# Performance work log

Measured on AMD Instinct MI355X. Metric: run time of the kernel, lower is better.

## Reference

```python
import jax, jax.numpy as jnp
import numpy as np

E = 1024   # embedding_dim
H = 16     # num_head
D = 64     # dim_head (E == H*D)
R = 8      # LoRA rank
BATCH = 2
SEQ = 2048
EPS = 1e-6


def setup_inputs() -> dict:
    key = jax.random.key(0)
    ks = jax.random.split(key, 16)
    s = 0.02
    return {
        "y": jax.random.normal(ks[0], (BATCH, SEQ, E), jnp.float32),
        "Wqkv": jax.random.normal(ks[1], (3 * E, E), jnp.float32) * s,
        "bqkv": jax.random.normal(ks[2], (3 * E,), jnp.float32) * s,
        "Wmsa": jax.random.normal(ks[3], (E, E), jnp.float32) * s,
        "Bq": jax.random.normal(ks[4], (E, R), jnp.float32) * s,
        "Aq": jax.random.normal(ks[5], (R, E), jnp.float32) * s,
        "Bk": jax.random.normal(ks[6], (E, R), jnp.float32) * s,
        "Ak": jax.random.normal(ks[7], (R, E), jnp.float32) * s,
        "Bv": jax.random.normal(ks[8], (E, R), jnp.float32) * s,
        "Av": jax.random.normal(ks[9], (R, E), jnp.float32) * s,
        "Bo": jax.random.normal(ks[10], (E, R), jnp.float32) * s,
        "Ao": jax.random.normal(ks[11], (R, E), jnp.float32) * s,
        "gamma": jnp.ones((E,), jnp.float32),
        "beta": jnp.zeros((E,), jnp.float32),
        "i": 0,
    }


def reference(y, Wqkv, bqkv, Wmsa, Bq, Aq, Bk, Ak, Bv, Av, Bo, Ao, gamma, beta, i):
    B, S, En = y.shape
    # fused QKV projection: nn.Linear -> y @ W.T + b
    qkv = (y @ Wqkv.T + bqkv).reshape(B, S, 3, H, D).transpose(2, 0, 3, 1, 4)
    Q, K, V = qkv[0], qkv[1], qkv[2]          # each [B,H,S,D]

    def lora_delta(Bw, Aw):
        # torch: y @ (B.weight @ A.weight), reshaped to heads
        return (y @ (Bw @ Aw)).reshape(B, S, H, D).transpose(0, 2, 1, 3)

    Q = Q + lora_delta(Bq, Aq)
    K = K + lora_delta(Bk, Ak)
    V = V + lora_delta(Bv, Av)

    scale = jnp.asarray(np.sqrt(D), y.dtype)
    scores = jnp.einsum('bhqd,bhkd->bhqk', Q, K) / scale
    attn = jax.nn.softmax(scores, axis=-1)
    o = jnp.einsum('bhqk,bhkd->bhqd', attn, V)          # [B,H,S,D]
    o = o.transpose(0, 2, 1, 3).reshape(B, S, H * D)    # [B,S,E]

    msa = o @ Wmsa.T + o @ (Bo @ Ao)
    res = msa + y

    mu = jnp.mean(res, axis=-1, keepdims=True)
    var = jnp.var(res, axis=-1, keepdims=True)
    return (res - mu) * jax.lax.rsqrt(var + EPS) * gamma + beta
```

## Files before the change

kernel.cpp:

```cpp
#include <hip/hip_runtime.h>
#include <hip/hip_bf16.h>
#include <stdint.h>

typedef __attribute__((ext_vector_type(8))) short short8;
typedef __attribute__((ext_vector_type(4))) float f32x4;

typedef const __attribute__((address_space(1))) void gv_t;
typedef __attribute__((address_space(3))) void lv_t;

#define SCQ 0.18033688011112042f

__device__ __forceinline__ void gl_lds16(const void* g, void* l) {
    __builtin_amdgcn_global_load_lds((gv_t*)g, (lv_t*)l, 16, 0, 0);
}

__device__ __forceinline__ unsigned short f2bf(float f) {
    union { float f; unsigned int u; } v; v.f = f;
    unsigned int r = v.u + 0x7fffu + ((v.u >> 16) & 1u);
    return (unsigned short)(r >> 16);
}

__device__ __forceinline__ unsigned int pack2bf(float a, float b) {
    union { __hip_bfloat162 h2; unsigned int u; } cv;
    cv.h2 = __float22bfloat162_rn(make_float2(a, b));
    return cv.u;
}

__device__ __forceinline__ f32x4 zero4() { f32x4 z = {0.f, 0.f, 0.f, 0.f}; return z; }

__global__ void k_prep(const float* __restrict__ y,
                       const float* __restrict__ Wqkv, const float* __restrict__ Wmsa,
                       const float* __restrict__ Bq, const float* __restrict__ Aq,
                       const float* __restrict__ Bk, const float* __restrict__ Ak,
                       const float* __restrict__ Bv, const float* __restrict__ Av,
                       const float* __restrict__ Bo, const float* __restrict__ Ao,
                       unsigned short* __restrict__ wout, unsigned short* __restrict__ yb) {
    const int bid = blockIdx.x;
    if (bid < 16384) {
        int idx = bid * 256 + threadIdx.x;
        int n = idx >> 10, k = idx & 1023;
        int sel = n >> 10, n0 = n & 1023;
        const float* Bp = (sel == 0) ? Bq : (sel == 1) ? Bk : (sel == 2) ? Bv : Bo;
        const float* Ap = (sel == 0) ? Aq : (sel == 1) ? Ak : (sel == 2) ? Av : Ao;
        float acc = (sel < 3) ? Wqkv[idx] : Wmsa[idx - 3145728];
        #pragma unroll
        for (int r = 0; r < 8; ++r) acc += Bp[k * 8 + r] * Ap[r * 1024 + n0];
        wout[idx] = f2bf(acc * ((sel == 0) ? SCQ : 1.0f));
    } else {
        int i = ((bid - 16384) * 256 + threadIdx.x) * 4;
        float4 v = *(const float4*)(y + i);
        union { unsigned short u[4]; uint2 w; } o;
        o.u[0] = f2bf(v.x); o.u[1] = f2bf(v.y); o.u[2] = f2bf(v.z); o.u[3] = f2bf(v.w);
        *(uint2*)(yb + i) = o.w;
    }
}

template <int TM, int EPI, int MINW>
__global__ __launch_bounds__(256, MINW) void k_gemm(const unsigned short* __restrict__ Ag,
                                                    const unsigned short* __restrict__ Bg,
                                                    const float* __restrict__ bias,
                                                    const float* __restrict__ yres,
                                                    unsigned short* __restrict__ vtg,
                                                    void* __restrict__ Cout,
                                                    int M, int N, int K) {
    constexpr int WAVES_N = 256 / TM;
    constexpr int WN = TM / 2;
    constexpr int NI = WN / 16;
    constexpr int ACALLS = TM / 64;
    __shared__ unsigned short As[2][TM * 32];
    __shared__ unsigned short Bs[2][128 * 32];
    const int flat = threadIdx.x;
    const int m0 = blockIdx.y * TM, n0 = blockIdx.x * 128;
    const int lane = flat & 63, wave = flat >> 6;
    const int l16 = lane & 15, quad = lane >> 4;
    const int wm = (wave / WAVES_N) * 64, wn = (wave % WAVES_N) * WN;

    f32x4 acc[4][NI];
    #pragma unroll
    for (int mi = 0; mi < 4; ++mi)
        #pragma unroll
        for (int ni = 0; ni < NI; ++ni) acc[mi][ni] = zero4();

    const unsigned short* ap = Ag + (size_t)(m0 + (flat >> 2)) * K + (flat & 3) * 8;
    const unsigned short* bp = Bg + (size_t)(n0 + (flat >> 2)) * K + (flat & 3) * 8;
    const size_t rstep = (size_t)64 * K;

    #pragma unroll
    for (int c = 0; c < ACALLS; ++c) gl_lds16(ap + c * rstep, &As[0][c * 2048 + flat * 8]);
    gl_lds16(bp,         &Bs[0][flat * 8]);
    gl_lds16(bp + rstep, &Bs[0][2048 + flat * 8]);
    ap += 32; bp += 32;
    __syncthreads();

    for (int k0 = 0; k0 < K; k0 += 32) {
        const int cur = (k0 >> 5) & 1;
        if (k0 + 32 < K) {
            const int nxt = cur ^ 1;
            #pragma unroll
            for (int c = 0; c < ACALLS; ++c) gl_lds16(ap + c * rstep, &As[nxt][c * 2048 + flat * 8]);
            gl_lds16(bp,         &Bs[nxt][flat * 8]);
            gl_lds16(bp + rstep, &Bs[nxt][2048 + flat * 8]);
            ap += 32; bp += 32;
        }

        short8 af[4], bfr[NI];
        #pragma unroll
        for (int i = 0; i < 4; ++i) af[i] = *(const short8*)&As[cur][(wm + i * 16 + l16) * 32 + quad * 8];
        #pragma unroll
        for (int i = 0; i < NI; ++i) bfr[i] = *(const short8*)&Bs[cur][(wn + i * 16 + l16) * 32 + quad * 8];
        #pragma unroll
        for (int mi = 0; mi < 4; ++mi)
            #pragma unroll
            for (int ni = 0; ni < NI; ++ni)
                acc[mi][ni] = __builtin_amdgcn_mfma_f32_16x16x32_bf16(af[mi], bfr[ni], acc[mi][ni], 0, 0, 0);

        __syncthreads();
    }

    if (EPI == 0) {
        unsigned short* C = (unsigned short*)Cout;
        if (n0 < 2048) {
            #pragma unroll
            for (int ni = 0; ni < NI; ++ni) {
                int col = n0 + wn + ni * 16 + l16;
                float bv = bias[col] * ((col < 1024) ? SCQ : 1.0f);
                #pragma unroll
                for (int mi = 0; mi < 4; ++mi) {
                    int row = m0 + wm + mi * 16 + quad * 4;
                    #pragma unroll
                    for (int r = 0; r < 4; ++r)
                        C[(size_t)(row + r) * N + col] = f2bf(acc[mi][ni][r] + bv);
                }
            }
        } else {
            #pragma unroll
            for (int ni = 0; ni < NI; ++ni) {
                int col = n0 + wn + ni * 16 + l16;
                float bv = bias[col];
                int hh = (col - 2048) >> 6, dd = col & 63;
                unsigned short* vrow0 = vtg + (size_t)(hh * 64 + dd) * 2048;
                #pragma unroll
                for (int mi = 0; mi < 4; ++mi) {
                    int row = m0 + wm + mi * 16 + quad * 4;
                    int bb = row >> 11, ss = row & 2047;
                    uint2 w;
                    w.x = pack2bf(acc[mi][ni][0] + bv, acc[mi][ni][1] + bv);
                    w.y = pack2bf(acc[mi][ni][2] + bv, acc[mi][ni][3] + bv);
                    *(uint2*)(vrow0 + (size_t)bb * 2097152 + ss) = w;
                }
            }
        }
    } else {
        float* C = (float*)Cout;
        #pragma unroll
        for (int ni = 0; ni < NI; ++ni) {
            int col = n0 + wn + ni * 16 + l16;
            #pragma unroll
            for (int mi = 0; mi < 4; ++mi) {
                int row = m0 + wm + mi * 16 + quad * 4;
                #pragma unroll
                for (int r = 0; r < 4; ++r)
                    C[(size_t)(row + r) * N + col] = acc[mi][ni][r] + yres[(size_t)(row + r) * N + col];
            }
        }
    }
}

__global__ __launch_bounds__(256, 3) void k_attn(const unsigned short* __restrict__ qkv,
                                                 const unsigned short* __restrict__ vtg,
                                                 unsigned short* __restrict__ o) {
    __shared__ unsigned short LDS[24576];
    unsigned short* Qs = LDS;
    unsigned short* Ks0 = LDS + 8192;
    unsigned short* Vt0 = LDS + 16384;

    const int t = threadIdx.x;
    const int lane = t & 63, wave = t >> 6;
    const int l16 = lane & 15, quad = lane >> 4;
    const int l8 = l16 & 7;
    const int q0 = blockIdx.x * 128;
    const int h = blockIdx.y, b = blockIdx.z;

    const unsigned short* qbase = qkv + (size_t)(b * 2048) * 3072 + h * 64;
    const unsigned short* kbase = qbase + 1024;
    const unsigned short* vtbase = vtg + (size_t)((b * 16 + h) * 64) * 2048;

    #pragma unroll
    for (int i = 0; i < 4; ++i) {
        int B = i * 256 + t;
        int row = B >> 3, c = (B & 7) ^ (row & 7);
        gl_lds16(qbase + (size_t)(q0 + row) * 3072 + c * 8, &Qs[B * 8]);
    }

    const int B0 = t, B1 = t + 256;
    const int r0 = B0 >> 3, c0 = (B0 & 7) ^ (r0 & 7);
    const int r1 = B1 >> 3, c1 = (B1 & 7) ^ (r1 & 7);
    const unsigned short* kp0 = kbase + (size_t)r0 * 3072 + c0 * 8;
    const unsigned short* kp1 = kbase + (size_t)r1 * 3072 + c1 * 8;
    const unsigned short* vp0 = vtbase + (size_t)r0 * 2048 + c0 * 8;
    const unsigned short* vp1 = vtbase + (size_t)r1 * 2048 + c1 * 8;

    gl_lds16(kp0, &Ks0[B0 * 8]);
    gl_lds16(kp1, &Ks0[B1 * 8]);
    gl_lds16(vp0, &Vt0[B0 * 8]);
    gl_lds16(vp1, &Vt0[B1 * 8]);
    kp0 += 64 * 3072; kp1 += 64 * 3072; vp0 += 64; vp1 += 64;

    __syncthreads();

    short8 qf[2][2];
    #pragma unroll
    for (int ni = 0; ni < 2; ++ni)
        #pragma unroll
        for (int kk = 0; kk < 2; ++kk)
            qf[ni][kk] = *(const short8*)&Qs[(wave * 32 + ni * 16 + l16) * 64 + ((kk * 4 + quad) ^ l8) * 8];

    f32x4 acc_o[2][4];
    #pragma unroll
    for (int mo = 0; mo < 2; ++mo)
        #pragma unroll
        for (int nd = 0; nd < 4; ++nd) acc_o[mo][nd] = zero4();
    f32x4 acc_l[2] = {zero4(), zero4()};
    short8 ones;
    #pragma unroll
    for (int i = 0; i < 8; ++i) ones[i] = (short)0x3F80;

    for (int j = 0; j < 32; ++j) {
        const unsigned short* Ks = Ks0 + (j & 1) * 4096;
        const unsigned short* Vt = Vt0 + (j & 1) * 4096;

        if (j < 31) {
            unsigned short* Kn = Ks0 + ((j + 1) & 1) * 4096;
            unsigned short* Vn = Vt0 + ((j + 1) & 1) * 4096;
            gl_lds16(kp0, &Kn[B0 * 8]);
            gl_lds16(kp1, &Kn[B1 * 8]);
            gl_lds16(vp0, &Vn[B0 * 8]);
            gl_lds16(vp1, &Vn[B1 * 8]);
            kp0 += 64 * 3072; kp1 += 64 * 3072; vp0 += 64; vp1 += 64;
        }

        f32x4 sacc[4][2];
        #pragma unroll
        for (int mi = 0; mi < 4; ++mi)
            #pragma unroll
            for (int ni = 0; ni < 2; ++ni) sacc[mi][ni] = zero4();
        #pragma unroll
        for (int kk = 0; kk < 2; ++kk)
            #pragma unroll
            for (int mi = 0; mi < 4; ++mi) {
                short8 kf = *(const short8*)&Ks[(mi * 16 + l16) * 64 + ((kk * 4 + quad) ^ l8) * 8];
                #pragma unroll
                for (int ni = 0; ni < 2; ++ni)
                    sacc[mi][ni] = __builtin_amdgcn_mfma_f32_16x16x32_bf16(kf, qf[ni][kk], sacc[mi][ni], 0, 0, 0);
            }

        short8 pf[2][2];
        #pragma unroll
        for (int ni = 0; ni < 2; ++ni)
            #pragma unroll
            for (int kk = 0; kk < 2; ++kk) {
                float e00 = __builtin_amdgcn_exp2f(sacc[2 * kk][ni][0]);
                float e01 = __builtin_amdgcn_exp2f(sacc[2 * kk][ni][1]);
                float e02 = __builtin_amdgcn_exp2f(sacc[2 * kk][ni][2]);
                float e03 = __builtin_amdgcn_exp2f(sacc[2 * kk][ni][3]);
                float e10 = __builtin_amdgcn_exp2f(sacc[2 * kk + 1][ni][0]);
                float e11 = __builtin_amdgcn_exp2f(sacc[2 * kk + 1][ni][1]);
                float e12 = __builtin_amdgcn_exp2f(sacc[2 * kk + 1][ni][2]);
                float e13 = __builtin_amdgcn_exp2f(sacc[2 * kk + 1][ni][3]);
                unsigned int a0 = pack2bf(e00, e01);
                unsigned int b0 = pack2bf(e10, e11);
                unsigned int a1 = pack2bf(e02, e03);
                unsigned int b1 = pack2bf(e12, e13);
                asm volatile("v_permlane32_swap_b32 %0, %1\n\t"
                             "v_permlane16_swap_b32 %0, %1"
                             : "+v"(a0), "+v"(b0));
                asm volatile("v_permlane32_swap_b32 %0, %1\n\t"
                             "v_permlane16_swap_b32 %0, %1"
                             : "+v"(a1), "+v"(b1));
                union { unsigned int u[4]; short8 s; } cv;
                cv.u[0] = a0; cv.u[1] = a1; cv.u[2] = b0; cv.u[3] = b1;
                pf[ni][kk] = cv.s;
            }

        #pragma unroll
        for (int kk = 0; kk < 2; ++kk) {
            #pragma unroll
            for (int mo = 0; mo < 2; ++mo)
                acc_l[mo] = __builtin_amdgcn_mfma_f32_16x16x32_bf16(pf[mo][kk], ones, acc_l[mo], 0, 0, 0);
            #pragma unroll
            for (int nd = 0; nd < 4; ++nd) {
                short8 vf = *(const short8*)&Vt[(nd * 16 + l16) * 64 + ((kk * 4 + quad) ^ l8) * 8];
                #pragma unroll
                for (int mo = 0; mo < 2; ++mo)
                    acc_o[mo][nd] = __builtin_amdgcn_mfma_f32_16x16x32_bf16(pf[mo][kk], vf, acc_o[mo][nd], 0, 0, 0);
            }
        }

        __syncthreads();
    }

    #pragma unroll
    for (int mo = 0; mo < 2; ++mo)
        #pragma unroll
        for (int rr = 0; rr < 4; ++rr) {
            float inv = 1.0f / acc_l[mo][rr];
            int qg = q0 + wave * 32 + mo * 16 + quad * 4 + rr;
            size_t base = ((size_t)(b * 2048 + qg)) * 1024 + h * 64;
            #pragma unroll
            for (int nd = 0; nd < 4; ++nd)
                o[base + nd * 16 + l16] = f2bf(acc_o[mo][nd][rr] * inv);
        }
}

__global__ __launch_bounds__(256) void k_ln(const float* __restrict__ res,
                                            const float* __restrict__ g,
                                            const float* __restrict__ be,
                                            float* __restrict__ out) {
    __shared__ float red[8];
    const int row = blockIdx.x, t = threadIdx.x;
    const float* x = res + (size_t)row * 1024;
    float4 v = *(const float4*)(x + t * 4);
    float s = v.x + v.y + v.z + v.w;
    float sq = v.x * v.x + v.y * v.y + v.z * v.z + v.w * v.w;
    #pragma unroll
    for (int off = 32; off; off >>= 1) { s += __shfl_down(s, off); sq += __shfl_down(sq, off); }
    if ((t & 63) == 0) { red[t >> 6] = s; red[4 + (t >> 6)] = sq; }
    __syncthreads();
    float ts = red[0] + red[1] + red[2] + red[3];
    float tq = red[4] + red[5] + red[6] + red[7];
    float mu = ts * (1.f / 1024.f);
    float var = tq * (1.f / 1024.f) - mu * mu;
    float rstd = rsqrtf(var + 1e-6f);
    float4 gg = *(const float4*)(g + t * 4);
    float4 bb = *(const float4*)(be + t * 4);
    float4 ov;
    ov.x = (v.x - mu) * rstd * gg.x + bb.x;
    ov.y = (v.y - mu) * rstd * gg.y + bb.y;
    ov.z = (v.z - mu) * rstd * gg.z + bb.z;
    ov.w = (v.w - mu) * rstd * gg.w + bb.w;
    *(float4*)(out + (size_t)row * 1024 + t * 4) = ov;
}

extern "C" void kernel_launch(void* const* d_in, const int* in_sizes, int n_in,
                              void* d_out, int out_size, void* d_ws, size_t ws_size,
                              hipStream_t stream) {
    (void)in_sizes; (void)n_in; (void)out_size; (void)ws_size;
    const float* y    = (const float*)d_in[0];
    const float* Wqkv = (const float*)d_in[1];
    const float* bqkv = (const float*)d_in[2];
    const float* Wmsa = (const float*)d_in[3];
    const float* Bq = (const float*)d_in[4];
    const float* Aq = (const float*)d_in[5];
    const float* Bk = (const float*)d_in[6];
    const float* Ak = (const float*)d_in[7];
    const float* Bv = (const float*)d_in[8];
    const float* Av = (const float*)d_in[9];
    const float* Bo = (const float*)d_in[10];
    const float* Ao = (const float*)d_in[11];
    const float* gamma = (const float*)d_in[12];
    const float* beta  = (const float*)d_in[13];

    char* ws = (char*)d_ws;
    unsigned short* yb   = (unsigned short*)(ws);
    unsigned short* weq  = (unsigned short*)(ws + (8u  << 20));
    unsigned short* qkv  = (unsigned short*)(ws + (16u << 20));
    unsigned short* vtg  = (unsigned short*)(ws + (40u << 20));
    unsigned short* wem  = weq + 3145728;
    unsigned short* obuf = yb;
    float* res = (float*)qkv;

    k_prep<<<17408, 256, 0, stream>>>(y, Wqkv, Wmsa, Bq, Aq, Bk, Ak, Bv, Av, Bo, Ao, weq, yb);
    k_gemm<128, 0, 3><<<dim3(24, 32), 256, 0, stream>>>(yb, weq, bqkv, nullptr, vtg, (void*)qkv, 4096, 3072, 1024);
    k_attn<<<dim3(16, 16, 2), 256, 0, stream>>>(qkv, vtg, obuf);
    k_gemm<64, 1, 4><<<dim3(8, 64), 256, 0, stream>>>(obuf, wem, nullptr, y, nullptr, (void*)res, 4096, 1024, 1024);
    k_ln  <<<4096, 256, 0, stream>>>(res, gamma, beta, (float*)d_out);
}
```

Measured before the change: 212.5 us.

## Stage V-transpose via LDS, remap attention blocks per XCD, reuse LDS, wave-per-row layernorm

The QKV GEMM epilogue for V columns now stages results in a swizzled shared-memory tile and writes the transposed V with coalesced 16-byte stores. The previous path used scattered 8-byte stores. The attention kernel reuses the Q staging buffer for K/V to cut LDS to 32KB, and lowers its launch-bounds occupancy hint from 3 to 2. It also remaps a 1D grid so each XCD handles whole heads for better L2 locality of K/V, and simplifies the score MFMA chain. LayerNorm now assigns one wave per row without shared-memory reduction or block syncs, and launches four rows per block.

```diff
diff --git a/kernel.cpp b/kernel.cpp
--- a/kernel.cpp
+++ b/kernel.cpp
@@ -67,8 +67,10 @@
     constexpr int WN = TM / 2;
     constexpr int NI = WN / 16;
     constexpr int ACALLS = TM / 64;
-    __shared__ unsigned short As[2][TM * 32];
-    __shared__ unsigned short Bs[2][128 * 32];
+    constexpr int ASZ = 2 * TM * 32;
+    __shared__ unsigned short SH[ASZ + 2 * 128 * 32];
+    unsigned short* As0 = SH;
+    unsigned short* Bs0 = SH + ASZ;
     const int flat = threadIdx.x;
     const int m0 = blockIdx.y * TM, n0 = blockIdx.x * 128;
     const int lane = flat & 63, wave = flat >> 6;
@@ -86,9 +88,9 @@
     const size_t rstep = (size_t)64 * K;
 
     #pragma unroll
-    for (int c = 0; c < ACALLS; ++c) gl_lds16(ap + c * rstep, &As[0][c * 2048 + flat * 8]);
-    gl_lds16(bp,         &Bs[0][flat * 8]);
-    gl_lds16(bp + rstep, &Bs[0][2048 + flat * 8]);
+    for (int c = 0; c < ACALLS; ++c) gl_lds16(ap + c * rstep, &As0[c * 2048 + flat * 8]);
+    gl_lds16(bp,         &Bs0[flat * 8]);
+    gl_lds16(bp + rstep, &Bs0[2048 + flat * 8]);
     ap += 32; bp += 32;
     __syncthreads();
 
@@ -97,17 +99,17 @@
         if (k0 + 32 < K) {
             const int nxt = cur ^ 1;
             #pragma unroll
-            for (int c = 0; c < ACALLS; ++c) gl_lds16(ap + c * rstep, &As[nxt][c * 2048 + flat * 8]);
-            gl_lds16(bp,         &Bs[nxt][flat * 8]);
-            gl_lds16(bp + rstep, &Bs[nxt][2048 + flat * 8]);
+            for (int c = 0; c < ACALLS; ++c) gl_lds16(ap + c * rstep, &As0[nxt * TM * 32 + c * 2048 + flat * 8]);
+            gl_lds16(bp,         &Bs0[nxt * 4096 + flat * 8]);
+            gl_lds16(bp + rstep, &Bs0[nxt * 4096 + 2048 + flat * 8]);
             ap += 32; bp += 32;
         }
 
         short8 af[4], bfr[NI];
         #pragma unroll
-        for (int i = 0; i < 4; ++i) af[i] = *(const short8*)&As[cur][(wm + i * 16 + l16) * 32 + quad * 8];
-        #pragma unroll
-        for (int i = 0; i < NI; ++i) bfr[i] = *(const short8*)&Bs[cur][(wn + i * 16 + l16) * 32 + quad * 8];
+        for (int i = 0; i < 4; ++i) af[i] = *(const short8*)&As0[cur * TM * 32 + (wm + i * 16 + l16) * 32 + quad * 8];
+        #pragma unroll
+        for (int i = 0; i < NI; ++i) bfr[i] = *(const short8*)&Bs0[cur * 4096 + (wn + i * 16 + l16) * 32 + quad * 8];
         #pragma unroll
         for (int mi = 0; mi < 4; ++mi)
             #pragma unroll
@@ -133,20 +135,37 @@
                 }
             }
         } else {
-            #pragma unroll
-            for (int ni = 0; ni < NI; ++ni) {
-                int col = n0 + wn + ni * 16 + l16;
-                float bv = bias[col];
-                int hh = (col - 2048) >> 6, dd = col & 63;
-                unsigned short* vrow0 = vtg + (size_t)(hh * 64 + dd) * 2048;
+            if constexpr (TM == 128) {
                 #pragma unroll
-                for (int mi = 0; mi < 4; ++mi) {
-                    int row = m0 + wm + mi * 16 + quad * 4;
-                    int bb = row >> 11, ss = row & 2047;
-                    uint2 w;
-                    w.x = pack2bf(acc[mi][ni][0] + bv, acc[mi][ni][1] + bv);
-                    w.y = pack2bf(acc[mi][ni][2] + bv, acc[mi][ni][3] + bv);
-                    *(uint2*)(vrow0 + (size_t)bb * 2097152 + ss) = w;
+                for (int ni = 0; ni < NI; ++ni) {
+                    int c = wn + ni * 16 + l16;
+                    float bv = bias[n0 + c];
+                    int sw = (c & 7) << 3;
+                    #pragma unroll
+                    for (int mi = 0; mi < 4; ++mi) {
+                        int row = wm + mi * 16 + quad * 4;
+                        uint2 w;
+                        w.x = pack2bf(acc[mi][ni][0] + bv, acc[mi][ni][1] + bv);
+                        w.y = pack2bf(acc[mi][ni][2] + bv, acc[mi][ni][3] + bv);
+                        *(uint2*)&SH[c * 128 + (row ^ sw)] = w;
+                    }
+                }
+                __syncthreads();
+                const int bb = m0 >> 11, ss = m0 & 2047;
+                #pragma unroll
+                for (int p = 0; p < 4; ++p) {
+                    int c = p * 32 + (flat >> 3);
+                    int col = n0 + c;
+                    int hh = (col - 2048) >> 6, dd = col & 63;
+                    unsigned short* dst = vtg + (size_t)(hh * 64 + dd) * 2048
+                                              + (size_t)bb * 2097152 + ss;
+                    int sw = (c & 7) << 3;
+                    #pragma unroll
+                    for (int hf = 0; hf < 2; ++hf) {
+                        int off = hf * 64 + (flat & 7) * 8;
+                        uint4 v = *(const uint4*)&SH[c * 128 + (off ^ sw)];
+                        *(uint4*)(dst + off) = v;
+                    }
                 }
             }
         }
@@ -166,20 +185,24 @@
     }
 }
 
-__global__ __launch_bounds__(256, 3) void k_attn(const unsigned short* __restrict__ qkv,
+__global__ __launch_bounds__(256, 2) void k_attn(const unsigned short* __restrict__ qkv,
                                                  const unsigned short* __restrict__ vtg,
                                                  unsigned short* __restrict__ o) {
-    __shared__ unsigned short LDS[24576];
+    __shared__ unsigned short LDS[16384];
     unsigned short* Qs = LDS;
-    unsigned short* Ks0 = LDS + 8192;
-    unsigned short* Vt0 = LDS + 16384;
+    unsigned short* Ks0 = LDS;
+    unsigned short* Vt0 = LDS + 8192;
 
     const int t = threadIdx.x;
     const int lane = t & 63, wave = t >> 6;
     const int l16 = lane & 15, quad = lane >> 4;
     const int l8 = l16 & 7;
-    const int q0 = blockIdx.x * 128;
-    const int h = blockIdx.y, b = blockIdx.z;
+    const int id = blockIdx.x;
+    const int xcd = id & 7, loc = id >> 3;
+    const int qb = loc & 15;
+    const int P = xcd + 8 * (loc >> 4);
+    const int h = P & 15, b = P >> 4;
+    const int q0 = qb * 128;
 
     const unsigned short* qbase = qkv + (size_t)(b * 2048) * 3072 + h * 64;
     const unsigned short* kbase = qbase + 1024;
@@ -200,30 +223,35 @@
     const unsigned short* vp0 = vtbase + (size_t)r0 * 2048 + c0 * 8;
     const unsigned short* vp1 = vtbase + (size_t)r1 * 2048 + c1 * 8;
 
+    __syncthreads();
+
+    short8 qf[2][2];
+    #pragma unroll
+    for (int ni = 0; ni < 2; ++ni)
+        #pragma unroll
+        for (int kk = 0; kk < 2; ++kk)
+            qf[ni][kk] = *(const short8*)&Qs[(wave * 32 + ni * 16 + l16) * 64 + ((kk * 4 + quad) ^ l8) * 8];
+
+    __syncthreads();
+
     gl_lds16(kp0, &Ks0[B0 * 8]);
     gl_lds16(kp1, &Ks0[B1 * 8]);
     gl_lds16(vp0, &Vt0[B0 * 8]);
     gl_lds16(vp1, &Vt0[B1 * 8]);
     kp0 += 64 * 3072; kp1 += 64 * 3072; vp0 += 64; vp1 += 64;
 
-    __syncthreads();
-
-    short8 qf[2][2];
-    #pragma unroll
-    for (int ni = 0; ni < 2; ++ni)
-        #pragma unroll
-        for (int kk = 0; kk < 2; ++kk)
-            qf[ni][kk] = *(const short8*)&Qs[(wave * 32 + ni * 16 + l16) * 64 + ((kk * 4 + quad) ^ l8) * 8];
-
     f32x4 acc_o[2][4];
     #pragma unroll
     for (int mo = 0; mo < 2; ++mo)
         #pragma unroll
         for (int nd = 0; nd < 4; ++nd) acc_o[mo][nd] = zero4();
     f32x4 acc_l[2] = {zero4(), zero4()};
+    const f32x4 Z4 = zero4();
     short8 ones;
     #pragma unroll
     for (int i = 0; i < 8; ++i) ones[i] = (short)0x3F80;
+
+    __syncthreads();
 
     for (int j = 0; j < 32; ++j) {
         const unsigned short* Ks = Ks0 + (j & 1) * 4096;
@@ -241,18 +269,15 @@
 
         f32x4 sacc[4][2];
         #pragma unroll
-        for (int mi = 0; mi < 4; ++mi)
-            #pragma unroll
-            for (int ni = 0; ni < 2; ++ni) sacc[mi][ni] = zero4();
-        #pragma unroll
-        for (int kk = 0; kk < 2; ++kk)
-            #pragma unroll
-            for (int mi = 0; mi < 4; ++mi) {
-                short8 kf = *(const short8*)&Ks[(mi * 16 + l16) * 64 + ((kk * 4 + quad) ^ l8) * 8];
-                #pragma unroll
-                for (int ni = 0; ni < 2; ++ni)
-                    sacc[mi][ni] = __builtin_amdgcn_mfma_f32_16x16x32_bf16(kf, qf[ni][kk], sacc[mi][ni], 0, 0, 0);
-            }
+        for (int mi = 0; mi < 4; ++mi) {
+            short8 kf0 = *(const short8*)&Ks[(mi * 16 + l16) * 64 + ((0 + quad) ^ l8) * 8];
+            short8 kf1 = *(const short8*)&Ks[(mi * 16 + l16) * 64 + ((4 + quad) ^ l8) * 8];
+            #pragma unroll
+            for (int ni = 0; ni < 2; ++ni) {
+                sacc[mi][ni] = __builtin_amdgcn_mfma_f32_16x16x32_bf16(kf0, qf[ni][0], Z4, 0, 0, 0);
+                sacc[mi][ni] = __builtin_amdgcn_mfma_f32_16x16x32_bf16(kf1, qf[ni][1], sacc[mi][ni], 0, 0, 0);
+            }
+        }
 
         short8 pf[2][2];
         #pragma unroll
@@ -316,29 +341,35 @@
                                             const float* __restrict__ g,
                                             const float* __restrict__ be,
                                             float* __restrict__ out) {
-    __shared__ float red[8];
-    const int row = blockIdx.x, t = threadIdx.x;
+    const int row = blockIdx.x * 4 + (threadIdx.x >> 6);
+    const int lane = threadIdx.x & 63;
     const float* x = res + (size_t)row * 1024;
-    float4 v = *(const float4*)(x + t * 4);
-    float s = v.x + v.y + v.z + v.w;
-    float sq = v.x * v.x + v.y * v.y + v.z * v.z + v.w * v.w;
+    float4 v[4];
+    float s = 0.f, sq = 0.f;
+    #pragma unroll
+    for (int i = 0; i < 4; ++i) {
+        v[i] = *(const float4*)(x + i * 256 + lane * 4);
+        s  += v[i].x + v[i].y + v[i].z + v[i].w;
+        sq += v[i].x * v[i].x + v[i].y * v[i].y + v[i].z * v[i].z + v[i].w * v[i].w;
+    }
     #pragma unroll
     for (int off = 32; off; off >>= 1) { s += __shfl_down(s, off); sq += __shfl_down(sq, off); }
-    if ((t & 63) == 0) { red[t >> 6] = s; red[4 + (t >> 6)] = sq; }
-    __syncthreads();
-    float ts = red[0] + red[1] + red[2] + red[3];
-    float tq = red[4] + red[5] + red[6] + red[7];
-    float mu = ts * (1.f / 1024.f);
-    float var = tq * (1.f / 1024.f) - mu * mu;
+    s = __shfl(s, 0); sq = __shfl(sq, 0);
+    float mu = s * (1.f / 1024.f);
+    float var = sq * (1.f / 1024.f) - mu * mu;
     float rstd = rsqrtf(var + 1e-6f);
-    float4 gg = *(const float4*)(g + t * 4);
-    float4 bb = *(const float4*)(be + t * 4);
-    float4 ov;
-    ov.x = (v.x - mu) * rstd * gg.x + bb.x;
-    ov.y = (v.y - mu) * rstd * gg.y + bb.y;
-    ov.z = (v.z - mu) * rstd * gg.z + bb.z;
-    ov.w = (v.w - mu) * rstd * gg.w + bb.w;
-    *(float4*)(out + (size_t)row * 1024 + t * 4) = ov;
+    float* orow = out + (size_t)row * 1024;
+    #pragma unroll
+    for (int i = 0; i < 4; ++i) {
+        float4 gg = *(const float4*)(g + i * 256 + lane * 4);
+        float4 bb = *(const float4*)(be + i * 256 + lane * 4);
+        float4 ov;
+        ov.x = (v[i].x - mu) * rstd * gg.x + bb.x;
+        ov.y = (v[i].y - mu) * rstd * gg.y + bb.y;
+        ov.z = (v[i].z - mu) * rstd * gg.z + bb.z;
+        ov.w = (v[i].w - mu) * rstd * gg.w + bb.w;
+        *(float4*)(orow + i * 256 + lane * 4) = ov;
+    }
 }
 
 extern "C" void kernel_launch(void* const* d_in, const int* in_sizes, int n_in,
@@ -371,7 +402,7 @@
 
     k_prep<<<17408, 256, 0, stream>>>(y, Wqkv, Wmsa, Bq, Aq, Bk, Ak, Bv, Av, Bo, Ao, weq, yb);
     k_gemm<128, 0, 3><<<dim3(24, 32), 256, 0, stream>>>(yb, weq, bqkv, nullptr, vtg, (void*)qkv, 4096, 3072, 1024);
-    k_attn<<<dim3(16, 16, 2), 256, 0, stream>>>(qkv, vtg, obuf);
+    k_attn<<<512, 256, 0, stream>>>(qkv, vtg, obuf);
     k_gemm<64, 1, 4><<<dim3(8, 64), 256, 0, stream>>>(obuf, wem, nullptr, y, nullptr, (void*)res, 4096, 1024, 1024);
-    k_ln  <<<4096, 256, 0, stream>>>(res, gamma, beta, (float*)d_out);
-}
+    k_ln  <<<1024, 256, 0, stream>>>(res, gamma, beta, (float*)d_out);
+}
```

After: 211.7 us. About the same (-0.4%).
